# Kernel optimization log

Measured on AMD Instinct MI355X. Metric: run time of the kernel, lower is better.

Reference implementation:

```python
import jax, jax.numpy as jnp
import numpy as np

N = 50000        # nodes
E = 640000       # edges
HID = 128        # hidden_channels
NF = 128         # num_filters
NG = 50          # num_gaussians
NL = 3           # num_interactions
CUTOFF = 5.0
NGRAPHS = 64
NZ = 100         # atom-type vocab (PyG SchNet embedding size)


def _ssp(x):
    # ShiftedSoftplus
    return jax.nn.softplus(x) - jnp.log(2.0).astype(x.dtype)


def setup_inputs() -> dict:
    key = jax.random.key(0)
    ks = jax.random.split(key, 16)
    z = jax.random.randint(ks[0], (N,), 0, NZ, dtype=jnp.int32)
    pos = jax.random.uniform(ks[1], (N, 3), jnp.float32)
    src = jax.random.randint(ks[2], (E,), 0, N)
    off = jax.random.randint(ks[3], (E,), 1, N)
    dst = (src + off) % N  # guarantee no self-loops (nonzero distances)
    edge_index = jnp.stack([src, dst]).astype(jnp.int64)
    batch_index = jnp.sort(jax.random.randint(ks[4], (N,), 0, NGRAPHS, dtype=jnp.int32))
    s = 0.05
    emb = jax.random.normal(ks[5], (NZ, HID), jnp.float32) * s
    mlp_w1 = jax.random.normal(ks[6], (NL, NG, NF), jnp.float32) * s
    mlp_b1 = jnp.zeros((NL, NF), jnp.float32)
    mlp_w2 = jax.random.normal(ks[7], (NL, NF, NF), jnp.float32) * s
    mlp_b2 = jnp.zeros((NL, NF), jnp.float32)
    conv1_w = jax.random.normal(ks[8], (NL, HID, NF), jnp.float32) * s   # CFConv.lin1 (no bias)
    conv2_w = jax.random.normal(ks[9], (NL, NF, HID), jnp.float32) * s   # CFConv.lin2
    conv2_b = jnp.zeros((NL, HID), jnp.float32)
    lin_w = jax.random.normal(ks[10], (NL, HID, HID), jnp.float32) * s   # InteractionBlock.lin
    lin_b = jnp.zeros((NL, HID), jnp.float32)
    out1_w = jax.random.normal(ks[11], (HID, HID // 2), jnp.float32) * s
    out1_b = jnp.zeros((HID // 2,), jnp.float32)
    out2_w = jax.random.normal(ks[12], (HID // 2, 1), jnp.float32) * s
    out2_b = jnp.zeros((1,), jnp.float32)
    return dict(z=z, pos=pos, edge_index=edge_index, batch_index=batch_index,
                emb=emb, mlp_w1=mlp_w1, mlp_b1=mlp_b1, mlp_w2=mlp_w2, mlp_b2=mlp_b2,
                conv1_w=conv1_w, conv2_w=conv2_w, conv2_b=conv2_b,
                lin_w=lin_w, lin_b=lin_b,
                out1_w=out1_w, out1_b=out1_b, out2_w=out2_w, out2_b=out2_b)


def reference(z, pos, edge_index, batch_index, emb, mlp_w1, mlp_b1, mlp_w2, mlp_b2,
              conv1_w, conv2_w, conv2_b, lin_w, lin_b, out1_w, out1_b, out2_w, out2_b):
    src, dst = edge_index[0], edge_index[1]
    diff = pos[dst] - pos[src]                      # [E,3]
    d = jnp.sqrt(jnp.sum(diff * diff, axis=-1))     # [E]

    # Gaussian smearing (GaussianSmearing(0, cutoff, NG))
    offset = jnp.linspace(0.0, CUTOFF, NG).astype(pos.dtype)
    coeff = -0.5 / (CUTOFF / (NG - 1)) ** 2
    edge_attr = jnp.exp(coeff * (d[:, None] - offset) ** 2)  # [E,NG]

    # SmoothBumpEnvelope: exp(1 - 1/(1 - (d/cutoff)^2)) for d < cutoff, else 0
    srel = d / CUTOFF
    inside = srel < 1.0
    denom = jnp.where(inside, 1.0 - srel * srel, 1.0)
    env = jnp.where(inside, jnp.exp(1.0 - 1.0 / denom), 0.0)
    edge_attr = edge_attr * env[:, None]

    # Cosine cutoff applied inside PyG CFConv
    C = 0.5 * (jnp.cos(d * jnp.pi / CUTOFF) + 1.0)  # [E]

    h = emb[z]  # [N,HID]
    for l in range(NL):
        # edge filter MLP: Linear -> ShiftedSoftplus -> Linear, then * cosine cutoff
        W = _ssp(edge_attr @ mlp_w1[l] + mlp_b1[l]) @ mlp_w2[l] + mlp_b2[l]  # [E,NF]
        W = W * C[:, None]
        xf = h @ conv1_w[l]                                   # [N,NF]
        msg = xf[src] * W                                     # gather + modulate
        agg = jax.ops.segment_sum(msg, dst, num_segments=N)   # scatter-add to targets
        xf = agg @ conv2_w[l] + conv2_b[l]                    # [N,HID]
        xf = _ssp(xf)
        h = h + (xf @ lin_w[l] + lin_b[l])                    # residual interaction

    h = _ssp(h @ out1_w + out1_b)
    e_atom = h @ out2_w + out2_b                              # [N,1]
    return jax.ops.segment_sum(e_atom, batch_index, num_segments=NGRAPHS)  # [NGRAPHS,1]
```

## Files before the change

kernel.cpp:

```cpp
#include <hip/hip_runtime.h>
#include <math.h>

#define N_NODES 50000
#define N_EDGES 640000
#define HID 128
#define NL 3
#define NGRAPHS 64
#define NT 4096
#define TPTS 8
#define DMAX 1.7330f
#define NPAD 50176
#define NTILES 1563
#define NWT 3125

typedef __attribute__((ext_vector_type(8))) short bf16x8;
typedef __attribute__((ext_vector_type(4))) float f32x4;

__device__ __align__(16) float g_h  [N_NODES * HID];
__device__ __align__(16) unsigned short g_xfb [N_NODES * HID];
__device__ __align__(16) unsigned short g_aggb[N_NODES * HID];
__device__ __align__(16) float g_table[NL * NT * HID];
__device__ __align__(16) unsigned short g_wT[9 * HID * HID];
__device__ __align__(16) int   g_cnt[NPAD];
__device__ __align__(16) int   g_ex [NPAD];
__device__ __align__(16) int   g_row[NPAD];
__device__ __align__(16) int   g_part[256];
__device__ __align__(16) int   g_ssrc[N_EDGES];
__device__ __align__(16) int   g_sidx[N_EDGES];
__device__ __align__(16) float g_gout[NGRAPHS];

__device__ __forceinline__ unsigned short f2bfbits(float x){
    union { float f; unsigned int i; } v; v.f = x;
    unsigned int lsb = (v.i >> 16) & 1;
    v.i += 0x7fff + lsb;
    return (unsigned short)(v.i >> 16);
}
__device__ __forceinline__ float bf2f(unsigned short u){
    union { unsigned int i; float f; } v; v.i = ((unsigned int)u) << 16; return v.f;
}
__device__ __forceinline__ float sspf(float x){
    return fmaxf(x, 0.0f) + log1pf(__expf(-fabsf(x))) - 0.69314718055994530942f;
}

__global__ __launch_bounds__(256) void zero_cnt_kernel(){
    int i = blockIdx.x * 256 + threadIdx.x;
    g_cnt[i] = 0;
    if (blockIdx.x == 0 && threadIdx.x < NGRAPHS) g_gout[threadIdx.x] = 0.0f;
}
__global__ __launch_bounds__(256) void hist_kernel(const int* __restrict__ dst){
    int e = blockIdx.x * 256 + threadIdx.x;
    atomicAdd(&g_cnt[dst[e]], 1);
}
__global__ __launch_bounds__(256) void scan1_kernel(){
    __shared__ int s[256];
    int b = blockIdx.x, t = threadIdx.x, i = b * 256 + t;
    int c = g_cnt[i];
    s[t] = c; __syncthreads();
    #pragma unroll
    for (int off = 1; off < 256; off <<= 1){
        int v = (t >= off) ? s[t - off] : 0; __syncthreads();
        s[t] += v; __syncthreads();
    }
    g_ex[i] = s[t] - c;
    if (t == 255) g_part[b] = s[255];
}
__global__ __launch_bounds__(256) void scan2_kernel(){
    __shared__ int s[256];
    int t = threadIdx.x;
    s[t] = (t < 196) ? g_part[t] : 0; __syncthreads();
    #pragma unroll
    for (int off = 1; off < 256; off <<= 1){
        int v = (t >= off) ? s[t - off] : 0; __syncthreads();
        s[t] += v; __syncthreads();
    }
    g_part[t] = s[t];
}
__global__ __launch_bounds__(256) void scan3_kernel(){
    int b = blockIdx.x, i = b * 256 + threadIdx.x;
    g_row[i] = g_ex[i] + (b > 0 ? g_part[b - 1] : 0);
}
__global__ __launch_bounds__(256) void scatter_kernel(
    const float* __restrict__ pos, const int* __restrict__ src,
    const int* __restrict__ dst)
{
    int e = blockIdx.x * 256 + threadIdx.x;
    int sv = src[e], dv = dst[e];
    float dx = pos[3*dv]   - pos[3*sv];
    float dy = pos[3*dv+1] - pos[3*sv+1];
    float dz = pos[3*dv+2] - pos[3*sv+2];
    float d = sqrtf(dx*dx + dy*dy + dz*dz);
    int p = atomicAdd(&g_row[dv], 1);
    g_ssrc[p] = sv;
    g_sidx[p] = (int)(d * ((float)(NT - 1) / DMAX) + 0.5f);
}

__global__ __launch_bounds__(128) void table_kernel(
    const float* __restrict__ w1g, const float* __restrict__ b1g,
    const float* __restrict__ w2g, const float* __restrict__ b2g)
{
    int bid = blockIdx.x;
    int l = bid / (NT / TPTS);
    int pt0 = (bid % (NT / TPTS)) * TPTS;
    int n = threadIdx.x;
    __shared__ __align__(16) float w1s[50 * 128];
    __shared__ float ea[TPTS][50];
    __shared__ float tm[TPTS][128];
    __shared__ float Cv[TPTS];
    for (int i = n; i < 50 * 128; i += 128) w1s[i] = w1g[(size_t)l * 50 * 128 + i];
    if (n < 50){
        const float step = 5.0f / 49.0f;
        #pragma unroll
        for (int p = 0; p < TPTS; p++){
            float d = (pt0 + p) * (DMAX / (float)(NT - 1));
            float srel = d * 0.2f;
            float env = expf(1.0f - 1.0f / (1.0f - srel * srel));
            float dd = d - step * (float)n;
            ea[p][n] = expf((-0.5f / (step * step)) * dd * dd) * env;
        }
    }
    if (n < TPTS){
        float d = (pt0 + n) * (DMAX / (float)(NT - 1));
        Cv[n] = 0.5f * (cosf(d * 0.62831853071795864769f) + 1.0f);
    }
    __syncthreads();
    float b1v = b1g[l * 128 + n];
    #pragma unroll
    for (int p = 0; p < TPTS; p++){
        float acc = b1v;
        #pragma unroll 10
        for (int k = 0; k < 50; k++) acc = fmaf(ea[p][k], w1s[k * 128 + n], acc);
        tm[p][n] = sspf(acc);
    }
    __syncthreads();
    float b2v = b2g[l * 128 + n];
    float acc2[TPTS];
    #pragma unroll
    for (int p = 0; p < TPTS; p++) acc2[p] = b2v;
    const float* w2 = w2g + (size_t)l * 128 * 128;
    for (int k = 0; k < 128; k++){
        float wv = w2[k * 128 + n];
        #pragma unroll
        for (int p = 0; p < TPTS; p++) acc2[p] = fmaf(tm[p][k], wv, acc2[p]);
    }
    #pragma unroll
    for (int p = 0; p < TPTS; p++)
        g_table[((size_t)l * NT + pt0 + p) * 128 + n] = acc2[p] * Cv[p];
}

__global__ __launch_bounds__(256) void wprep_kernel(
    const float* __restrict__ c1, const float* __restrict__ c2,
    const float* __restrict__ lwp)
{
    int gid = blockIdx.x * 256 + threadIdx.x;
    int mat = gid >> 14, r = gid & 16383;
    int n = r & 127, k = r >> 7;
    int l = mat / 3, w = mat % 3;
    const float* base = (w == 0 ? c1 : w == 1 ? c2 : lwp) + (size_t)l * HID * HID;
    g_wT[(size_t)mat * HID * HID + n * 128 + k] = f2bfbits(base[k * 128 + n]);
}

__global__ __launch_bounds__(256) void conv1_kernel(
    const int* __restrict__ z, const float* __restrict__ emb)
{
    __shared__ __align__(16) unsigned short a_s[32 * 128];
    __shared__ int zl[32];
    int tid = threadIdx.x;
    int wave = tid >> 6, lane = tid & 63, quad = lane >> 4, l16 = lane & 15;
    int mtile = (wave & 1) * 16, nbase = (wave >> 1) * 64;
    for (int t = blockIdx.x; t < NTILES; t += gridDim.x){
        int base = t * 32;
        __syncthreads();
        if (tid < 32) zl[tid] = (base + tid < N_NODES) ? z[base + tid] : 0;
        __syncthreads();
        for (int i = tid; i < 512; i += 256){
            int nn = i >> 4, c = i & 15, node = base + nn;
            int phys = c ^ (nn & 15);
            uint4 q = {0u, 0u, 0u, 0u};
            if (node < N_NODES){
                const float* p = &emb[(size_t)zl[nn] * 128 + c * 8];
                float4 f0 = *(const float4*)p;
                float4 f1 = *(const float4*)(p + 4);
                *(float4*)&g_h[(size_t)node * 128 + c * 8]     = f0;
                *(float4*)&g_h[(size_t)node * 128 + c * 8 + 4] = f1;
                q.x = (unsigned int)f2bfbits(f0.x) | ((unsigned int)f2bfbits(f0.y) << 16);
                q.y = (unsigned int)f2bfbits(f0.z) | ((unsigned int)f2bfbits(f0.w) << 16);
                q.z = (unsigned int)f2bfbits(f1.x) | ((unsigned int)f2bfbits(f1.y) << 16);
                q.w = (unsigned int)f2bfbits(f1.z) | ((unsigned int)f2bfbits(f1.w) << 16);
            }
            *(uint4*)&a_s[nn * 128 + phys * 8] = q;
        }
        __syncthreads();
        bf16x8 av[4];
        int arow = mtile + l16;
        #pragma unroll
        for (int ks = 0; ks < 4; ks++){
            int phys = (ks * 4 + quad) ^ (arow & 15);
            av[ks] = *(const bf16x8*)&a_s[arow * 128 + phys * 8];
        }
        f32x4 acc[4] = {};
        #pragma unroll
        for (int nt = 0; nt < 4; nt++){
            int n = nbase + nt * 16 + l16;
            #pragma unroll
            for (int ks = 0; ks < 4; ks++){
                bf16x8 bv = *(const bf16x8*)&g_wT[n * 128 + ks * 32 + quad * 8];
                acc[nt] = __builtin_amdgcn_mfma_f32_16x16x32_bf16(av[ks], bv, acc[nt], 0, 0, 0);
            }
        }
        #pragma unroll
        for (int nt = 0; nt < 4; nt++){
            int n = nbase + nt * 16 + l16;
            #pragma unroll
            for (int r = 0; r < 4; r++){
                int node = base + mtile + quad * 4 + r;
                if (node < N_NODES)
                    g_xfb[(size_t)node * 128 + n] = f2bfbits(acc[nt][r]);
            }
        }
    }
}

__global__ __launch_bounds__(256) void fused_kernel(
    int l, const float* __restrict__ bias2, const float* __restrict__ biasl,
    int skip3)
{
    __shared__ __align__(16) unsigned short t_sl[4][16 * 128];
    int tid = threadIdx.x;
    int wave = tid >> 6, lane = tid & 63, quad = lane >> 4, l16 = lane & 15;
    const unsigned short* c2  = g_wT + (size_t)(l * 3 + 1) * HID * HID;
    const unsigned short* lw  = g_wT + (size_t)(l * 3 + 2) * HID * HID;
    const unsigned short* c1n = g_wT + (size_t)((l + 1) * 3) * HID * HID;
    unsigned short* ts = t_sl[wave];

    int wt = blockIdx.x * 4 + wave;
    if (wt >= NWT) return;
    int base = wt * 16;

    float b2r[8], blr[8];
    #pragma unroll
    for (int nt = 0; nt < 8; nt++){
        b2r[nt] = bias2[nt * 16 + l16];
        blr[nt] = biasl[nt * 16 + l16];
    }

    bf16x8 av[4];
    #pragma unroll
    for (int ks = 0; ks < 4; ks++)
        av[ks] = *(const bf16x8*)&g_aggb[(size_t)(base + l16) * 128 + ks * 32 + quad * 8];
    f32x4 acc[8] = {};
    #pragma unroll
    for (int nt = 0; nt < 8; nt++){
        int n = nt * 16 + l16;
        #pragma unroll
        for (int ks = 0; ks < 4; ks++){
            bf16x8 bv = *(const bf16x8*)&c2[n * 128 + ks * 32 + quad * 8];
            acc[nt] = __builtin_amdgcn_mfma_f32_16x16x32_bf16(av[ks], bv, acc[nt], 0, 0, 0);
        }
    }
    #pragma unroll
    for (int nt = 0; nt < 8; nt++){
        int col = nt * 16 + l16;
        int c = col >> 3, sub = col & 7;
        #pragma unroll
        for (int r = 0; r < 4; r++){
            int row = quad * 4 + r;
            ts[row * 128 + ((c ^ row) & 15) * 8 + sub] =
                f2bfbits(sspf(acc[nt][r] + b2r[nt]));
        }
    }

    #pragma unroll
    for (int ks = 0; ks < 4; ks++){
        int phys = (ks * 4 + quad) ^ l16;
        av[ks] = *(const bf16x8*)&ts[l16 * 128 + phys * 8];
    }
    f32x4 acc2[8] = {};
    #pragma unroll
    for (int nt = 0; nt < 8; nt++){
        int n = nt * 16 + l16;
        #pragma unroll
        for (int ks = 0; ks < 4; ks++){
            bf16x8 bv = *(const bf16x8*)&lw[n * 128 + ks * 32 + quad * 8];
            acc2[nt] = __builtin_amdgcn_mfma_f32_16x16x32_bf16(av[ks], bv, acc2[nt], 0, 0, 0);
        }
    }
    #pragma unroll
    for (int nt = 0; nt < 8; nt++){
        int col = nt * 16 + l16;
        int c = col >> 3, sub = col & 7;
        #pragma unroll
        for (int r = 0; r < 4; r++){
            int row = quad * 4 + r;
            size_t o = (size_t)(base + row) * 128 + col;
            float hv = g_h[o] + acc2[nt][r] + blr[nt];
            g_h[o] = hv;
            if (!skip3)
                ts[row * 128 + ((c ^ row) & 15) * 8 + sub] = f2bfbits(hv);
        }
    }
    if (skip3) return;

    #pragma unroll
    for (int ks = 0; ks < 4; ks++){
        int phys = (ks * 4 + quad) ^ l16;
        av[ks] = *(const bf16x8*)&ts[l16 * 128 + phys * 8];
    }
    f32x4 acc3[8] = {};
    #pragma unroll
    for (int nt = 0; nt < 8; nt++){
        int n = nt * 16 + l16;
        #pragma unroll
        for (int ks = 0; ks < 4; ks++){
            bf16x8 bv = *(const bf16x8*)&c1n[n * 128 + ks * 32 + quad * 8];
            acc3[nt] = __builtin_amdgcn_mfma_f32_16x16x32_bf16(av[ks], bv, acc3[nt], 0, 0, 0);
        }
    }
    #pragma unroll
    for (int nt = 0; nt < 8; nt++){
        int col = nt * 16 + l16;
        #pragma unroll
        for (int r = 0; r < 4; r++){
            int row = quad * 4 + r;
            g_xfb[(size_t)(base + row) * 128 + col] = f2bfbits(acc3[nt][r]);
        }
    }
}

__global__ __launch_bounds__(256) void agg_kernel(int l){
    const float* __restrict__ T = g_table + (size_t)l * NT * 128;
    int tid = threadIdx.x;
    int grp = tid >> 5, n0 = (tid & 31) * 4;
    int v = blockIdx.x * 8 + grp;
    int e1 = g_row[v];
    int e0 = e1 - g_cnt[v];
    float a0 = 0.f, a1 = 0.f, a2 = 0.f, a3 = 0.f;
    int j = e0;
    for (; j + 4 <= e1; j += 4){
        int sA = g_ssrc[j],   sB = g_ssrc[j+1];
        int sC = g_ssrc[j+2], sD = g_ssrc[j+3];
        int iA = g_sidx[j],   iB = g_sidx[j+1];
        int iC = g_sidx[j+2], iD = g_sidx[j+3];
        float4 tA = *(const float4*)&T[(size_t)iA * 128 + n0];
        float4 tB = *(const float4*)&T[(size_t)iB * 128 + n0];
        float4 tC = *(const float4*)&T[(size_t)iC * 128 + n0];
        float4 tD = *(const float4*)&T[(size_t)iD * 128 + n0];
        ushort4 gA = *(const ushort4*)&g_xfb[(size_t)sA * 128 + n0];
        ushort4 gB = *(const ushort4*)&g_xfb[(size_t)sB * 128 + n0];
        ushort4 gC = *(const ushort4*)&g_xfb[(size_t)sC * 128 + n0];
        ushort4 gD = *(const ushort4*)&g_xfb[(size_t)sD * 128 + n0];
        a0 = fmaf(tA.x, bf2f(gA.x), a0); a1 = fmaf(tA.y, bf2f(gA.y), a1);
        a2 = fmaf(tA.z, bf2f(gA.z), a2); a3 = fmaf(tA.w, bf2f(gA.w), a3);
        a0 = fmaf(tB.x, bf2f(gB.x), a0); a1 = fmaf(tB.y, bf2f(gB.y), a1);
        a2 = fmaf(tB.z, bf2f(gB.z), a2); a3 = fmaf(tB.w, bf2f(gB.w), a3);
        a0 = fmaf(tC.x, bf2f(gC.x), a0); a1 = fmaf(tC.y, bf2f(gC.y), a1);
        a2 = fmaf(tC.z, bf2f(gC.z), a2); a3 = fmaf(tC.w, bf2f(gC.w), a3);
        a0 = fmaf(tD.x, bf2f(gD.x), a0); a1 = fmaf(tD.y, bf2f(gD.y), a1);
        a2 = fmaf(tD.z, bf2f(gD.z), a2); a3 = fmaf(tD.w, bf2f(gD.w), a3);
    }
    for (; j < e1; j++){
        int s = g_ssrc[j], i0 = g_sidx[j];
        float4 t0 = *(const float4*)&T[(size_t)i0 * 128 + n0];
        ushort4 g = *(const ushort4*)&g_xfb[(size_t)s * 128 + n0];
        a0 = fmaf(t0.x, bf2f(g.x), a0); a1 = fmaf(t0.y, bf2f(g.y), a1);
        a2 = fmaf(t0.z, bf2f(g.z), a2); a3 = fmaf(t0.w, bf2f(g.w), a3);
    }
    ushort4 o;
    o.x = f2bfbits(a0); o.y = f2bfbits(a1); o.z = f2bfbits(a2); o.w = f2bfbits(a3);
    *(ushort4*)&g_aggb[(size_t)v * 128 + n0] = o;
}

__global__ __launch_bounds__(256) void head_kernel(
    const float* __restrict__ w1g, const float* __restrict__ b1g,
    const float* __restrict__ w2g, const float* __restrict__ b2g,
    const int* __restrict__ batch)
{
    __shared__ __align__(16) float w1h[128 * 64];
    __shared__ __align__(16) float w2h[64];
    __shared__ __align__(16) float b1h[64];
    __shared__ __align__(16) float hrow[4][128];
    __shared__ float part[NGRAPHS];
    int tid = threadIdx.x;
    for (int i = tid; i < 128 * 64 / 4; i += 256)
        *(float4*)&w1h[i * 4] = *(const float4*)&w1g[i * 4];
    if (tid < 64){ w2h[tid] = w2g[tid]; b1h[tid] = b1g[tid]; }
    if (tid < NGRAPHS) part[tid] = 0.0f;
    float sb2 = b2g[0];
    __syncthreads();
    int wave = tid >> 6, lane = tid & 63;
    for (int nb = blockIdx.x * 4; nb < N_NODES; nb += gridDim.x * 4){
        int node = nb + wave;
        __syncthreads();
        if (node < N_NODES){
            hrow[wave][lane]      = g_h[(size_t)node * 128 + lane];
            hrow[wave][64 + lane] = g_h[(size_t)node * 128 + 64 + lane];
        }
        __syncthreads();
        if (node < N_NODES){
            float acc = b1h[lane];
            #pragma unroll 8
            for (int k = 0; k < 128; k++)
                acc = fmaf(hrow[wave][k], w1h[k * 64 + lane], acc);
            acc = sspf(acc) * w2h[lane];
            #pragma unroll
            for (int off = 32; off > 0; off >>= 1) acc += __shfl_down(acc, off, 64);
            if (lane == 0) atomicAdd(&part[batch[node]], acc + sb2);
        }
    }
    __syncthreads();
    if (tid < NGRAPHS && part[tid] != 0.0f)
        __hip_atomic_fetch_add(&g_gout[tid], part[tid],
                               __ATOMIC_RELAXED, __HIP_MEMORY_SCOPE_AGENT);
}

__global__ void store_kernel(float* __restrict__ out){
    int i = threadIdx.x;
    if (i < NGRAPHS) out[i] = g_gout[i];
}

extern "C" void kernel_launch(void* const* d_in, const int* in_sizes, int n_in,
                              void* d_out, int out_size, void* d_ws, size_t ws_size,
                              hipStream_t stream)
{
    const int* z       = (const int*)d_in[0];
    const float* pos   = (const float*)d_in[1];
    const int* ei      = (const int*)d_in[2];
    const int* src = ei;
    const int* dst = ei + N_EDGES;
    const int* batch   = (const int*)d_in[3];
    const float* emb     = (const float*)d_in[4];
    const float* mlp_w1  = (const float*)d_in[5];
    const float* mlp_b1  = (const float*)d_in[6];
    const float* mlp_w2  = (const float*)d_in[7];
    const float* mlp_b2  = (const float*)d_in[8];
    const float* conv1_w = (const float*)d_in[9];
    const float* conv2_w = (const float*)d_in[10];
    const float* conv2_b = (const float*)d_in[11];
    const float* lin_w   = (const float*)d_in[12];
    const float* lin_b   = (const float*)d_in[13];
    const float* out1_w  = (const float*)d_in[14];
    const float* out1_b  = (const float*)d_in[15];
    const float* out2_w  = (const float*)d_in[16];
    const float* out2_b  = (const float*)d_in[17];
    (void)d_ws; (void)ws_size; (void)in_sizes; (void)n_in; (void)out_size;

    zero_cnt_kernel<<<196, 256, 0, stream>>>();
    hist_kernel<<<2500, 256, 0, stream>>>(dst);
    scan1_kernel<<<196, 256, 0, stream>>>();
    scan2_kernel<<<1, 256, 0, stream>>>();
    scan3_kernel<<<196, 256, 0, stream>>>();
    scatter_kernel<<<2500, 256, 0, stream>>>(pos, src, dst);
    table_kernel<<<NL * (NT / TPTS), 128, 0, stream>>>(mlp_w1, mlp_b1, mlp_w2, mlp_b2);
    wprep_kernel<<<576, 256, 0, stream>>>(conv1_w, conv2_w, lin_w);

    conv1_kernel<<<NTILES, 256, 0, stream>>>(z, emb);
    for (int l = 0; l < NL; l++){
        agg_kernel<<<6250, 256, 0, stream>>>(l);
        fused_kernel<<<(NWT + 3) / 4, 256, 0, stream>>>(l, conv2_b + (size_t)l * HID,
                                                        lin_b + (size_t)l * HID, l == NL - 1);
    }

    head_kernel<<<512, 256, 0, stream>>>(out1_w, out1_b, out2_w, out2_b, batch);
    store_kernel<<<1, 64, 0, stream>>>((float*)d_out);
}
```

Before: 601.3 us.

## Rewrite output head MLP with bf16 MFMA tiles over 16-node blocks

The head kernel previously computed each node's 128x64 output projection with scalar FMAs, one wave per node, staging weights and rows in shared memory. It now gives each wave a 16-node tile, converts h to bf16 and uses 16x16x32 bf16 MFMA against a pre-transposed bf16 copy of out1_w written by a new small prep kernel. Per-row softplus and dot with out2_w are reduced with lane shuffles before the per-graph atomics. Rounding h and the weights to bf16 adds error to the final energies.

```diff
diff --git a/kernel.cpp b/kernel.cpp
--- a/kernel.cpp
+++ b/kernel.cpp
@@ -21,6 +21,7 @@
 __device__ __align__(16) unsigned short g_aggb[N_NODES * HID];
 __device__ __align__(16) float g_table[NL * NT * HID];
 __device__ __align__(16) unsigned short g_wT[9 * HID * HID];
+__device__ __align__(16) unsigned short g_w1hT[64 * HID];
 __device__ __align__(16) int   g_cnt[NPAD];
 __device__ __align__(16) int   g_ex [NPAD];
 __device__ __align__(16) int   g_row[NPAD];
@@ -157,6 +158,12 @@
     int l = mat / 3, w = mat % 3;
     const float* base = (w == 0 ? c1 : w == 1 ? c2 : lwp) + (size_t)l * HID * HID;
     g_wT[(size_t)mat * HID * HID + n * 128 + k] = f2bfbits(base[k * 128 + n]);
+}
+
+__global__ __launch_bounds__(256) void wprep2_kernel(const float* __restrict__ w1g){
+    int gid = blockIdx.x * 256 + threadIdx.x;
+    int n = gid & 63, k = gid >> 6;
+    g_w1hT[n * 128 + k] = f2bfbits(w1g[k * 64 + n]);
 }
 
 __global__ __launch_bounds__(256) void conv1_kernel(
@@ -370,40 +377,66 @@
 }
 
 __global__ __launch_bounds__(256) void head_kernel(
-    const float* __restrict__ w1g, const float* __restrict__ b1g,
-    const float* __restrict__ w2g, const float* __restrict__ b2g,
-    const int* __restrict__ batch)
-{
-    __shared__ __align__(16) float w1h[128 * 64];
-    __shared__ __align__(16) float w2h[64];
-    __shared__ __align__(16) float b1h[64];
-    __shared__ __align__(16) float hrow[4][128];
+    const float* __restrict__ b1g, const float* __restrict__ w2g,
+    const float* __restrict__ b2g, const int* __restrict__ batch)
+{
     __shared__ float part[NGRAPHS];
     int tid = threadIdx.x;
-    for (int i = tid; i < 128 * 64 / 4; i += 256)
-        *(float4*)&w1h[i * 4] = *(const float4*)&w1g[i * 4];
-    if (tid < 64){ w2h[tid] = w2g[tid]; b1h[tid] = b1g[tid]; }
+    int wave = tid >> 6, lane = tid & 63, quad = lane >> 4, l16 = lane & 15;
     if (tid < NGRAPHS) part[tid] = 0.0f;
+    __syncthreads();
     float sb2 = b2g[0];
-    __syncthreads();
-    int wave = tid >> 6, lane = tid & 63;
-    for (int nb = blockIdx.x * 4; nb < N_NODES; nb += gridDim.x * 4){
-        int node = nb + wave;
-        __syncthreads();
-        if (node < N_NODES){
-            hrow[wave][lane]      = g_h[(size_t)node * 128 + lane];
-            hrow[wave][64 + lane] = g_h[(size_t)node * 128 + 64 + lane];
-        }
-        __syncthreads();
-        if (node < N_NODES){
-            float acc = b1h[lane];
-            #pragma unroll 8
-            for (int k = 0; k < 128; k++)
-                acc = fmaf(hrow[wave][k], w1h[k * 64 + lane], acc);
-            acc = sspf(acc) * w2h[lane];
-            #pragma unroll
-            for (int off = 32; off > 0; off >>= 1) acc += __shfl_down(acc, off, 64);
-            if (lane == 0) atomicAdd(&part[batch[node]], acc + sb2);
+
+    int wt = blockIdx.x * 4 + wave;
+    if (wt < NWT){
+        int base = wt * 16;
+        float b1r[4], w2r[4];
+        #pragma unroll
+        for (int nt = 0; nt < 4; nt++){
+            b1r[nt] = b1g[nt * 16 + l16];
+            w2r[nt] = w2g[nt * 16 + l16];
+        }
+        bf16x8 av[4];
+        #pragma unroll
+        for (int ks = 0; ks < 4; ks++){
+            const float* p = &g_h[(size_t)(base + l16) * 128 + ks * 32 + quad * 8];
+            float4 f0 = *(const float4*)p;
+            float4 f1 = *(const float4*)(p + 4);
+            union { unsigned int u[4]; bf16x8 v; } pk;
+            pk.u[0] = (unsigned int)f2bfbits(f0.x) | ((unsigned int)f2bfbits(f0.y) << 16);
+            pk.u[1] = (unsigned int)f2bfbits(f0.z) | ((unsigned int)f2bfbits(f0.w) << 16);
+            pk.u[2] = (unsigned int)f2bfbits(f1.x) | ((unsigned int)f2bfbits(f1.y) << 16);
+            pk.u[3] = (unsigned int)f2bfbits(f1.z) | ((unsigned int)f2bfbits(f1.w) << 16);
+            av[ks] = pk.v;
+        }
+        f32x4 acc[4] = {};
+        #pragma unroll
+        for (int nt = 0; nt < 4; nt++){
+            int n = nt * 16 + l16;
+            #pragma unroll
+            for (int ks = 0; ks < 4; ks++){
+                bf16x8 bv = *(const bf16x8*)&g_w1hT[n * 128 + ks * 32 + quad * 8];
+                acc[nt] = __builtin_amdgcn_mfma_f32_16x16x32_bf16(av[ks], bv, acc[nt], 0, 0, 0);
+            }
+        }
+        float srow[4];
+        #pragma unroll
+        for (int r = 0; r < 4; r++){
+            float s = 0.0f;
+            #pragma unroll
+            for (int nt = 0; nt < 4; nt++)
+                s += sspf(acc[nt][r] + b1r[nt]) * w2r[nt];
+            #pragma unroll
+            for (int off = 1; off < 16; off <<= 1)
+                s += __shfl_xor(s, off, 64);
+            srow[r] = s;
+        }
+        if (l16 == 0){
+            #pragma unroll
+            for (int r = 0; r < 4; r++){
+                int node = base + quad * 4 + r;
+                atomicAdd(&part[batch[node]], srow[r] + sb2);
+            }
         }
     }
     __syncthreads();
@@ -451,6 +484,7 @@
     scatter_kernel<<<2500, 256, 0, stream>>>(pos, src, dst);
     table_kernel<<<NL * (NT / TPTS), 128, 0, stream>>>(mlp_w1, mlp_b1, mlp_w2, mlp_b2);
     wprep_kernel<<<576, 256, 0, stream>>>(conv1_w, conv2_w, lin_w);
+    wprep2_kernel<<<32, 256, 0, stream>>>(out1_w);
 
     conv1_kernel<<<NTILES, 256, 0, stream>>>(z, emb);
     for (int l = 0; l < NL; l++){
@@ -459,6 +493,6 @@
                                                         lin_b + (size_t)l * HID, l == NL - 1);
     }
 
-    head_kernel<<<512, 256, 0, stream>>>(out1_w, out1_b, out2_w, out2_b, batch);
+    head_kernel<<<(NWT + 3) / 4, 256, 0, stream>>>(out1_b, out2_w, out2_b, batch);
     store_kernel<<<1, 64, 0, stream>>>((float*)d_out);
 }
```

Result: faster. 555.7 us (-7.6%).
